# Kernel optimization log

Measured on AMD Instinct MI355X. Metric: run time of the kernel, lower is better.

The kernel has to match this reference:

```python
import jax, jax.numpy as jnp
import numpy as np

VOCAB, EMB, HID, OUT = 32000, 512, 1024, 8
B, S = 128, 512


def setup_inputs() -> dict:
    key = jax.random.key(0)
    ks = jax.random.split(key, 7)
    sequence_ids = jax.random.randint(ks[0], (B, S), 0, VOCAB)
    scale = 0.02
    emb = jax.random.normal(ks[1], (VOCAB, EMB), dtype=jnp.float32) * scale
    W_ih = jax.random.normal(ks[2], (4 * HID, EMB), dtype=jnp.float32) * scale
    W_hh = jax.random.normal(ks[3], (4 * HID, HID), dtype=jnp.float32) * scale
    b = jax.random.normal(ks[4], (4 * HID,), dtype=jnp.float32) * scale
    W_out = jax.random.normal(ks[5], (OUT, HID), dtype=jnp.float32) * scale
    b_out = jax.random.normal(ks[6], (OUT,), dtype=jnp.float32) * scale
    return {"sequence_ids": sequence_ids, "emb": emb, "W_ih": W_ih, "W_hh": W_hh,
            "b": b, "W_out": W_out, "b_out": b_out}


def reference(sequence_ids, emb, W_ih, W_hh, b, W_out, b_out):
    # embedding lookup: [B, S, E]
    x = emb[sequence_ids]
    Bb = x.shape[0]
    H = W_hh.shape[1]
    # precompute input projections for all timesteps at once: [S, B, 4H]
    xg = jnp.einsum('bse,ge->sbg', x, W_ih) + b

    def step(carry, xg_t):
        h, c = carry
        gates = xg_t + h @ W_hh.T  # [B, 4H]
        i, f, g, o = jnp.split(gates, 4, axis=-1)
        c = jax.nn.sigmoid(f) * c + jax.nn.sigmoid(i) * jnp.tanh(g)
        h = jax.nn.sigmoid(o) * jnp.tanh(c)
        return (h, c), None

    h0 = jnp.zeros((Bb, H), x.dtype)
    (h_last, _), _ = jax.lax.scan(step, (h0, h0), xg)
    # classifier on last hidden state: [B, OUT]
    return h_last @ W_out.T + b_out
```

## Files before the change

kernel.cpp:

```cpp
#include <hip/hip_runtime.h>
#include <cstdint>
#include <cstddef>

#define SEQ    512
#define BATCH  128
#define EMB    512
#define HID    1024
#define KTOT   1536
#define NOUT   8

#define RG     4
#define NBQ    64
#define NBLK   (RG*NBQ)
#define ROWS   32

typedef unsigned short u16;
typedef unsigned int   u32;
typedef unsigned long long u64;
typedef __attribute__((ext_vector_type(8))) __bf16 bf16x8;
typedef __attribute__((ext_vector_type(4))) float  f32x4;
typedef __attribute__((ext_vector_type(4))) float  float4v;
typedef __attribute__((ext_vector_type(4))) u16    u16x4;

#define OFF_X    0ull
#define SZ_X     ((size_t)SEQ*BATCH*EMB*2)
#define OFF_W    (OFF_X + SZ_X)
#define SZ_W     ((size_t)4*HID*KTOT*2)
#define OFF_RING (OFF_W + SZ_W)
#define SZ_RING  ((size_t)(SEQ+1)*BATCH*HID*2)
#define OFF_FW   (OFF_RING + SZ_RING)
#define SZ_FW    ((size_t)RG*NBQ*4*64)
#define WS_NEED  (OFF_FW + SZ_FW)

__device__ inline u16 f2b(float f) {
  uint32_t u = __builtin_bit_cast(uint32_t, f);
  u = u + 0x7FFFu + ((u >> 16) & 1u);
  return (u16)(u >> 16);
}
__device__ inline float b2f(u16 u) {
  uint32_t v = ((uint32_t)u) << 16;
  return __builtin_bit_cast(float, v);
}
__device__ inline float sigm(float x) { return 1.0f / (1.0f + __expf(-x)); }
__device__ inline float tanh_(float x) {
  x = fminf(fmaxf(x, -15.f), 15.f);
  float e = __expf(2.f * x);
  return (e - 1.f) / (e + 1.f);
}
__device__ inline f32x4 mfma16(bf16x8 a, bf16x8 b, f32x4 c) {
  return __builtin_amdgcn_mfma_f32_16x16x32_bf16(a, b, c, 0, 0, 0);
}

__global__ void embed_kernel(const int* __restrict__ ids,
                             const float* __restrict__ emb,
                             u16* __restrict__ x) {
  int bid = blockIdx.x;
  int t = bid >> 7, b = bid & 127;
  int idx = ids[b * SEQ + t];
  const float4v* src = (const float4v*)(emb + (size_t)idx * EMB);
  float4v v = src[threadIdx.x];
  u16x4 o;
  o.x = f2b(v.x); o.y = f2b(v.y); o.z = f2b(v.z); o.w = f2b(v.w);
  *(u16x4*)(x + (size_t)bid * EMB + threadIdx.x * 4) = o;
}

__global__ void wpack_kernel(const float* __restrict__ Wih,
                             const float* __restrict__ Whh,
                             u16* __restrict__ Wp) {
  int gc = blockIdx.x;
  int unit = gc >> 2, q = gc & 3;
  int row = q * HID + unit;
  u16* dst = Wp + (size_t)gc * KTOT;
  for (int k = threadIdx.x; k < KTOT; k += 256) {
    float v = (k < EMB) ? Wih[(size_t)row * EMB + k]
                        : Whh[(size_t)row * HID + (k - EMB)];
    dst[k] = f2b(v);
  }
}

__global__ __launch_bounds__(256, 1) void lstm_kernel(
    const u16* __restrict__ x,
    const u16* __restrict__ Wp,
    const float* __restrict__ bias,
    u16* __restrict__ ring,
    u32* __restrict__ fw)
{
  __shared__ float pacc[2][4][ROWS][68];

  const int tid  = threadIdx.x;
  const int bid  = blockIdx.x;
  const int rg   = bid & 3;
  const int nb   = bid >> 2;
  const int lane = tid & 63;
  const int kq   = tid >> 6;
  const int l15  = lane & 15;
  const int lhi  = lane >> 4;

  const int nxc  = (kq == 0) ? 12 : (kq == 1 ? 4 : 0);
  const int arow = rg * ROWS + l15;

  u32* fw_own = &fw[(((size_t)rg * NBQ + nb) * 4 + kq) * 16];
  const int pbase = (kq == 1) ? 0 : (kq == 2 ? 16 : 40);
  const int nflag = (kq == 1) ? 64 : 96;
  const u32* fp0 = &fw[(((size_t)rg * NBQ + pbase + (lane >> 2)) * 4 + (lane & 3)) * 16];
  const int  f2i = lane + 64;
  const u32* fp1 = (f2i < nflag)
      ? &fw[(((size_t)rg * NBQ + pbase + (f2i >> 2)) * 4 + (f2i & 3)) * 16]
      : fp0;

  bf16x8 wreg[12][4];
  {
    const int colbase = nb * 64;
    #pragma unroll
    for (int c = 0; c < 12; ++c)
      #pragma unroll
      for (int nt = 0; nt < 4; ++nt)
        wreg[c][nt] = *(const bf16x8*)(Wp
            + (size_t)(colbase + nt * 16 + l15) * KTOT
            + kq * 384 + c * 32 + lhi * 8);
  }

  const int urow = tid >> 3;
  const int up   = tid & 7;
  const int rowg = rg * ROWS + urow;
  float bs[2][4];
  #pragma unroll
  for (int k = 0; k < 2; ++k) {
    int ug = nb * 16 + 2 * up + k;
    #pragma unroll
    for (int q = 0; q < 4; ++q) bs[k][q] = bias[q * HID + ug];
  }
  float cst[2] = {0.f, 0.f};

  bf16x8 af[2][12];
  #pragma unroll
  for (int c = 0; c < 12; ++c)
    if (c < nxc) {
      #pragma unroll
      for (int mt = 0; mt < 2; ++mt)
        af[mt][c] = *(const bf16x8*)(x + (size_t)(arow + mt * 16) * EMB
                                     + kq * 384 + c * 32 + lhi * 8);
    }

  #pragma unroll 1
  for (int t = 0; t < SEQ; ++t) {
    const int pb = t & 1;

    f32x4 acc[2][4];
    #pragma unroll
    for (int mt = 0; mt < 2; ++mt)
      #pragma unroll
      for (int nt = 0; nt < 4; ++nt) acc[mt][nt] = (f32x4){0.f, 0.f, 0.f, 0.f};
    #pragma unroll
    for (int c = 0; c < 12; ++c)
      if (c < nxc) {
        #pragma unroll
        for (int mt = 0; mt < 2; ++mt)
          #pragma unroll
          for (int nt = 0; nt < 4; ++nt)
            acc[mt][nt] = mfma16(af[mt][c], wreg[c][nt], acc[mt][nt]);
      }

    if (t > 0 && kq > 0) {
      const u32 tgt = (u32)t;
      int bail = 0;
      for (;;) {
        u32 a = __hip_atomic_load(fp0, __ATOMIC_RELAXED, __HIP_MEMORY_SCOPE_AGENT);
        u32 b = __hip_atomic_load(fp1, __ATOMIC_RELAXED, __HIP_MEMORY_SCOPE_AGENT);
        if (__all((a >= tgt) & (b >= tgt))) break;
        if (++bail > (1 << 22)) break;
      }
      __asm__ __volatile__("" ::: "memory");
    }

    {
      const u16* hb = ring + (size_t)t * (BATCH * HID);
      #pragma unroll
      for (int c = 0; c < 12; ++c)
        if (c >= nxc) {
          #pragma unroll
          for (int mt = 0; mt < 2; ++mt)
            af[mt][c] = *(const bf16x8*)(hb + (size_t)(arow + mt * 16) * HID
                                         + (kq * 384 - 512 + c * 32) + lhi * 8);
        }
    }

    #pragma unroll
    for (int c = 0; c < 12; ++c)
      if (c >= nxc) {
        #pragma unroll
        for (int mt = 0; mt < 2; ++mt)
          #pragma unroll
          for (int nt = 0; nt < 4; ++nt)
            acc[mt][nt] = mfma16(af[mt][c], wreg[c][nt], acc[mt][nt]);
      }

    #pragma unroll
    for (int mt = 0; mt < 2; ++mt)
      #pragma unroll
      for (int nt = 0; nt < 4; ++nt)
        #pragma unroll
        for (int rr = 0; rr < 4; ++rr) {
          int row = mt * 16 + lhi * 4 + rr;
          int c   = nt * 16 + l15;
          int pc  = (c & ~7) | ((c ^ row) & 7);
          pacc[pb][kq][row][pc] = acc[mt][nt][rr];
        }
    __syncthreads();

    float s[2][4];
    #pragma unroll
    for (int k = 0; k < 2; ++k)
      #pragma unroll
      for (int q = 0; q < 4; ++q) s[k][q] = bs[k][q];
    #pragma unroll
    for (int k2 = 0; k2 < 4; ++k2)
      #pragma unroll
      for (int cl = 0; cl < 8; ++cl) {
        int pc = 8 * up + ((cl ^ urow) & 7);
        s[cl >> 2][cl & 3] += pacc[pb][k2][urow][pc];
      }

    {
      float hv2[2];
      #pragma unroll
      for (int k = 0; k < 2; ++k) {
        float cn = sigm(s[k][1]) * cst[k] + sigm(s[k][0]) * tanh_(s[k][2]);
        cst[k] = cn;
        hv2[k] = sigm(s[k][3]) * tanh_(cn);
      }
      u32 val = (u32)f2b(hv2[0]) | ((u32)f2b(hv2[1]) << 16);
      u32* dst = (u32*)(ring + (size_t)(t + 1) * (BATCH * HID)
                        + (size_t)rowg * HID + nb * 16 + 2 * up);
      asm volatile("global_store_dword %0, %1, off sc0 sc1"
                   :: "v"(dst), "v"(val) : "memory");
    }
    asm volatile("s_waitcnt vmcnt(0)" ::: "memory");

    if (t < SEQ - 1 && lane == 0) {
      __hip_atomic_store(fw_own, (u32)(t + 1), __ATOMIC_RELAXED,
                         __HIP_MEMORY_SCOPE_AGENT);
    }

    if (t < SEQ - 1) {
      const u16* xb = x + (size_t)(t + 1) * (BATCH * EMB);
      #pragma unroll
      for (int c = 0; c < 12; ++c)
        if (c < nxc) {
          #pragma unroll
          for (int mt = 0; mt < 2; ++mt)
            af[mt][c] = *(const bf16x8*)(xb + (size_t)(arow + mt * 16) * EMB
                                         + kq * 384 + c * 32 + lhi * 8);
        }
    }
  }
}

__global__ void head_kernel(const u16* __restrict__ h,
                            const float* __restrict__ Wout,
                            const float* __restrict__ bout,
                            float* __restrict__ out) {
  int b = blockIdx.x, l = threadIdx.x;
  float p[NOUT];
  #pragma unroll
  for (int o = 0; o < NOUT; ++o) p[o] = 0.f;
  for (int k = l; k < HID; k += 64) {
    float hv = b2f(h[(size_t)b * HID + k]);
    #pragma unroll
    for (int o = 0; o < NOUT; ++o) p[o] += hv * Wout[(size_t)o * HID + k];
  }
  #pragma unroll
  for (int o = 0; o < NOUT; ++o) {
    float v = p[o];
    #pragma unroll
    for (int off = 32; off > 0; off >>= 1) v += __shfl_down(v, off);
    if (l == 0) out[b * NOUT + o] = v + bout[o];
  }
}

__global__ void sentinel_kernel(float* out, int n) {
  int i = blockIdx.x * 256 + threadIdx.x;
  if (i < n) out[i] = 1e9f;
}

extern "C" void kernel_launch(void* const* d_in, const int* in_sizes, int n_in,
                              void* d_out, int out_size, void* d_ws, size_t ws_size,
                              hipStream_t stream) {
  const int*   ids  = (const int*)d_in[0];
  const float* emb  = (const float*)d_in[1];
  const float* Wih  = (const float*)d_in[2];
  const float* Whh  = (const float*)d_in[3];
  const float* bias = (const float*)d_in[4];
  const float* Wout = (const float*)d_in[5];
  const float* bout = (const float*)d_in[6];
  float* out = (float*)d_out;

  if (ws_size < WS_NEED) {
    sentinel_kernel<<<(out_size + 255) / 256, 256, 0, stream>>>(out, out_size);
    return;
  }

  char* ws = (char*)d_ws;
  u16* x    = (u16*)(ws + OFF_X);
  u16* Wp   = (u16*)(ws + OFF_W);
  u16* ring = (u16*)(ws + OFF_RING);
  u32* fwv  = (u32*)(ws + OFF_FW);

  hipMemsetAsync(ring, 0, (size_t)BATCH * HID * 2, stream);
  hipMemsetAsync(fwv, 0, SZ_FW, stream);

  embed_kernel<<<SEQ * BATCH, 128, 0, stream>>>(ids, emb, x);
  wpack_kernel<<<4 * HID, 256, 0, stream>>>(Wih, Whh, Wp);

  lstm_kernel<<<NBLK, 256, 0, stream>>>(x, Wp, bias, ring, fwv);

  head_kernel<<<BATCH, 64, 0, stream>>>(ring + (size_t)SEQ * BATCH * HID,
                                        Wout, bout, out);
}
```

Measured before the change: 2.707 ms.

## Split K evenly across waves so each handles x and h chunks uniformly

Before, the 1536-wide reduction was split so that wave 0 did only input (x) chunks, wave 1 did mixed chunks and waves 2-3 did only recurrent (h) chunks, which left the waits on recurrent state uneven. Now every wave takes 4 x-chunks (128 columns of EMB) and 8 h-chunks (256 columns of HID), and waits only on the 16 producer blocks that own its slice of h. This balances the critical-path work after the cross-block flag wait and halves the flag polling per wave. In exchange, all four waves now sit on the serial dependency, including wave 0 which previously never waited.

```diff
diff --git a/kernel.cpp b/kernel.cpp
--- a/kernel.cpp
+++ b/kernel.cpp
@@ -13,6 +13,8 @@
 #define NBQ    64
 #define NBLK   (RG*NBQ)
 #define ROWS   32
+
+#define KMAP(kq, c) ((c) < 4 ? ((kq)*128 + (c)*32) : (512 + (kq)*256 + ((c)-4)*32))
 
 typedef unsigned short u16;
 typedef unsigned int   u32;
@@ -96,17 +98,10 @@
   const int l15  = lane & 15;
   const int lhi  = lane >> 4;
 
-  const int nxc  = (kq == 0) ? 12 : (kq == 1 ? 4 : 0);
   const int arow = rg * ROWS + l15;
 
   u32* fw_own = &fw[(((size_t)rg * NBQ + nb) * 4 + kq) * 16];
-  const int pbase = (kq == 1) ? 0 : (kq == 2 ? 16 : 40);
-  const int nflag = (kq == 1) ? 64 : 96;
-  const u32* fp0 = &fw[(((size_t)rg * NBQ + pbase + (lane >> 2)) * 4 + (lane & 3)) * 16];
-  const int  f2i = lane + 64;
-  const u32* fp1 = (f2i < nflag)
-      ? &fw[(((size_t)rg * NBQ + pbase + (f2i >> 2)) * 4 + (f2i & 3)) * 16]
-      : fp0;
+  const u32* fp0 = &fw[(((size_t)rg * NBQ + 16 * kq + (lane >> 2)) * 4 + (lane & 3)) * 16];
 
   bf16x8 wreg[12][4];
   {
@@ -117,7 +112,7 @@
       for (int nt = 0; nt < 4; ++nt)
         wreg[c][nt] = *(const bf16x8*)(Wp
             + (size_t)(colbase + nt * 16 + l15) * KTOT
-            + kq * 384 + c * 32 + lhi * 8);
+            + KMAP(kq, c) + lhi * 8);
   }
 
   const int urow = tid >> 3;
@@ -134,13 +129,12 @@
 
   bf16x8 af[2][12];
   #pragma unroll
-  for (int c = 0; c < 12; ++c)
-    if (c < nxc) {
-      #pragma unroll
-      for (int mt = 0; mt < 2; ++mt)
-        af[mt][c] = *(const bf16x8*)(x + (size_t)(arow + mt * 16) * EMB
-                                     + kq * 384 + c * 32 + lhi * 8);
-    }
+  for (int c = 0; c < 4; ++c) {
+    #pragma unroll
+    for (int mt = 0; mt < 2; ++mt)
+      af[mt][c] = *(const bf16x8*)(x + (size_t)(arow + mt * 16) * EMB
+                                   + kq * 128 + c * 32 + lhi * 8);
+  }
 
   #pragma unroll 1
   for (int t = 0; t < SEQ; ++t) {
@@ -152,22 +146,19 @@
       #pragma unroll
       for (int nt = 0; nt < 4; ++nt) acc[mt][nt] = (f32x4){0.f, 0.f, 0.f, 0.f};
     #pragma unroll
-    for (int c = 0; c < 12; ++c)
-      if (c < nxc) {
-        #pragma unroll
-        for (int mt = 0; mt < 2; ++mt)
-          #pragma unroll
-          for (int nt = 0; nt < 4; ++nt)
-            acc[mt][nt] = mfma16(af[mt][c], wreg[c][nt], acc[mt][nt]);
-      }
-
-    if (t > 0 && kq > 0) {
+    for (int c = 0; c < 4; ++c)
+      #pragma unroll
+      for (int mt = 0; mt < 2; ++mt)
+        #pragma unroll
+        for (int nt = 0; nt < 4; ++nt)
+          acc[mt][nt] = mfma16(af[mt][c], wreg[c][nt], acc[mt][nt]);
+
+    if (t > 0) {
       const u32 tgt = (u32)t;
       int bail = 0;
       for (;;) {
         u32 a = __hip_atomic_load(fp0, __ATOMIC_RELAXED, __HIP_MEMORY_SCOPE_AGENT);
-        u32 b = __hip_atomic_load(fp1, __ATOMIC_RELAXED, __HIP_MEMORY_SCOPE_AGENT);
-        if (__all((a >= tgt) & (b >= tgt))) break;
+        if (__all(a >= tgt)) break;
         if (++bail > (1 << 22)) break;
       }
       __asm__ __volatile__("" ::: "memory");
@@ -176,24 +167,21 @@
     {
       const u16* hb = ring + (size_t)t * (BATCH * HID);
       #pragma unroll
-      for (int c = 0; c < 12; ++c)
-        if (c >= nxc) {
-          #pragma unroll
-          for (int mt = 0; mt < 2; ++mt)
-            af[mt][c] = *(const bf16x8*)(hb + (size_t)(arow + mt * 16) * HID
-                                         + (kq * 384 - 512 + c * 32) + lhi * 8);
-        }
-    }
-
-    #pragma unroll
-    for (int c = 0; c < 12; ++c)
-      if (c >= nxc) {
+      for (int c = 4; c < 12; ++c) {
         #pragma unroll
         for (int mt = 0; mt < 2; ++mt)
-          #pragma unroll
-          for (int nt = 0; nt < 4; ++nt)
-            acc[mt][nt] = mfma16(af[mt][c], wreg[c][nt], acc[mt][nt]);
-      }
+          af[mt][c] = *(const bf16x8*)(hb + (size_t)(arow + mt * 16) * HID
+                                       + kq * 256 + (c - 4) * 32 + lhi * 8);
+      }
+    }
+
+    #pragma unroll
+    for (int c = 4; c < 12; ++c)
+      #pragma unroll
+      for (int mt = 0; mt < 2; ++mt)
+        #pragma unroll
+        for (int nt = 0; nt < 4; ++nt)
+          acc[mt][nt] = mfma16(af[mt][c], wreg[c][nt], acc[mt][nt]);
 
     #pragma unroll
     for (int mt = 0; mt < 2; ++mt)
@@ -245,13 +233,12 @@
     if (t < SEQ - 1) {
       const u16* xb = x + (size_t)(t + 1) * (BATCH * EMB);
       #pragma unroll
-      for (int c = 0; c < 12; ++c)
-        if (c < nxc) {
-          #pragma unroll
-          for (int mt = 0; mt < 2; ++mt)
-            af[mt][c] = *(const bf16x8*)(xb + (size_t)(arow + mt * 16) * EMB
-                                         + kq * 384 + c * 32 + lhi * 8);
-        }
+      for (int c = 0; c < 4; ++c) {
+        #pragma unroll
+        for (int mt = 0; mt < 2; ++mt)
+          af[mt][c] = *(const bf16x8*)(xb + (size_t)(arow + mt * 16) * EMB
+                                       + kq * 128 + c * 32 + lhi * 8);
+      }
     }
   }
 }
```

Measured after the change: 2.619 ms (median of 2 runs). 3.2% less time.
